# Optimization experiments

Measured on AMD Instinct MI355X. Metric: run time of the kernel, lower is better.

Reference implementation:

```python
import jax, jax.numpy as jnp
import numpy as np
import math

B, S, F, D = 8, 2048, 1024, 1024
NEG = -1e9


def setup_inputs() -> dict:
    key = jax.random.key(0)
    ks = jax.random.split(key, 5)
    x = jax.random.normal(ks[0], (B, S, F), dtype=jnp.float32)
    r_mat = jax.random.normal(ks[1], (B, S, S), dtype=jnp.float32)
    # shared causal attention mask [S, S] (1 = keep, 0 = masked)
    attn_mask = jnp.tril(jnp.ones((S, S), dtype=jnp.float32))
    # per-batch padding mask [B, 1, S]: last 128 tokens of half the batch padded
    pad = jnp.ones((B, 1, S), dtype=jnp.float32)
    pad = pad.at[B // 2:, :, S - 128:].set(0.0)
    Wq = jax.random.normal(ks[2], (F, D), dtype=jnp.float32) / math.sqrt(F)
    Wk = jax.random.normal(ks[3], (F, D), dtype=jnp.float32) / math.sqrt(F)
    Wv = jax.random.normal(ks[4], (F, D), dtype=jnp.float32) / math.sqrt(F)
    return {"x": x, "r_mat": r_mat, "attn_mask": attn_mask, "pad_mask": pad,
            "Wq": Wq, "Wk": Wk, "Wv": Wv}


def reference(x, r_mat, attn_mask, pad_mask, Wq, Wk, Wv):
    scale = math.sqrt(x.shape[-1])  # original scales by sqrt(features)
    q = jnp.einsum('bsf,fd->bsd', x, Wq)
    k = jnp.einsum('bsf,fd->bsd', x, Wk)
    v = jnp.einsum('bsf,fd->bsd', x, Wv)
    scores = jnp.einsum('bsd,btd->bst', q, k) / scale  # [B, S, S]
    keep = (pad_mask != 0.0) & (attn_mask[None] != 0.0)  # [B, S, S] broadcast
    r = jnp.where(keep, r_mat, NEG)
    r = jax.nn.softmax(r, axis=-1)
    scores = jnp.where(keep, scores + r, NEG)
    prob = jax.nn.softmax(scores, axis=-1)
    return jnp.einsum('bst,btd->bsd', prob, v)
```

## Files before the change

kernel.cpp:

```cpp
#include <hip/hip_runtime.h>
#include <hip/hip_bf16.h>

#define B_ 8
#define S_ 2048
#define F_ 1024
#define D_ 1024
#define TRI_ 136
#define TELEM_ 16384

typedef unsigned short u16;
typedef float f32x4 __attribute__((ext_vector_type(4)));
typedef __bf16 bf16x8 __attribute__((ext_vector_type(8)));
typedef unsigned short u16x8 __attribute__((ext_vector_type(8)));

__device__ __forceinline__ u16 f2bf(float f) {
  union { float f; unsigned u; } v; v.f = f;
  unsigned r = v.u + 0x7fff + ((v.u >> 16) & 1);
  return (u16)(r >> 16);
}
__device__ __forceinline__ float bf2f(u16 b) {
  union { unsigned u; float f; } v; v.u = ((unsigned)b) << 16;
  return v.f;
}

__device__ __forceinline__ void stage16(const u16* g, u16* l) {
  __builtin_amdgcn_global_load_lds(
      (const __attribute__((address_space(1))) void*)g,
      (__attribute__((address_space(3))) void*)l, 16, 0, 0);
}

__device__ __forceinline__ int xcd_swz(int f, int n) {
  int per = n >> 3;
  return (f & 7) * per + (f >> 3);
}


__global__ __launch_bounds__(256) void prep(const float* __restrict__ x,
                                            const float* __restrict__ Wq,
                                            const float* __restrict__ Wk,
                                            const float* __restrict__ Wv,
                                            u16* __restrict__ xb,
                                            u16* __restrict__ Wt) {
  __shared__ float tile[32][33];
  if (blockIdx.x < 2048) {
    int n4 = (B_ * S_ * F_) / 4;
    for (int i = blockIdx.x * 256 + threadIdx.x; i < n4; i += 2048 * 256) {
      float4 v = ((const float4*)x)[i];
      ushort4 o;
      o.x = f2bf(v.x); o.y = f2bf(v.y); o.z = f2bf(v.z); o.w = f2bf(v.w);
      ((ushort4*)xb)[i] = o;
    }
  } else {
    int f = blockIdx.x - 2048;
    int z = f >> 10;
    int f2 = f & 1023;
    int f0 = (f2 >> 5) * 32, d0 = (f2 & 31) * 32;
    const float* W = (z == 0) ? Wq : ((z == 1) ? Wk : Wv);
    int tx = threadIdx.x & 31, ty = threadIdx.x >> 5;
    for (int i = 0; i < 4; i++)
      tile[ty + i * 8][tx] = W[(size_t)(f0 + ty + i * 8) * D_ + d0 + tx];
    __syncthreads();
    u16* o = Wt + (size_t)z * D_ * F_;
    for (int i = 0; i < 4; i++)
      o[(size_t)(d0 + ty + i * 8) * F_ + f0 + tx] = f2bf(tile[tx][ty + i * 8]);
  }
}

__global__ __launch_bounds__(256) void er_pass(const float* __restrict__ r,
                                               const float* __restrict__ pm,
                                               u16* __restrict__ er,
                                               float* __restrict__ rowsum) {
  int row = blockIdx.x;
  int b = row >> 11, s = row & 2047;
  if (threadIdx.x == 0) rowsum[row] = 0.f;
  const float4* rp = (const float4*)(r + (size_t)row * S_);
  const float4* pp = (const float4*)(pm + (size_t)b * S_);
  int nk = (s >> 2) + 1;
  int nw = ((s >> 7) + 1) << 5;
  float4 ev[8];
  float acc = 0.f;
  #pragma unroll
  for (int it = 0; it < 8; it++) {
    int i = threadIdx.x + it * 256;
    if (i < nk) {
      float4 rv = rp[i], pv = pp[i];
      int t0 = i << 2;
      float4 e;
      #pragma unroll
      for (int j = 0; j < 4; j++) {
        bool keep = (t0 + j <= s) && ((&pv.x)[j] != 0.f);
        (&e.x)[j] = keep ? __expf((&rv.x)[j] - 16.f) : 0.f;
        acc += (&e.x)[j];
      }
      ev[it] = e;
    }
  }
  for (int off = 1; off < 64; off <<= 1) acc += __shfl_xor(acc, off);
  __shared__ float wsum[4];
  int lane = threadIdx.x & 63, w = threadIdx.x >> 6;
  if (lane == 0) wsum[w] = acc;
  __syncthreads();
  float invr = 1.f / (wsum[0] + wsum[1] + wsum[2] + wsum[3]);
  int c = s >> 7, rin = s & 127;
  u16* tb = er + (size_t)(b * TRI_ + c * (c + 1) / 2) * TELEM_ + rin * 128;
  #pragma unroll
  for (int it = 0; it < 8; it++) {
    int i = threadIdx.x + it * 256;
    if (i < nw) {
      int t0 = i << 2;
      float4 pv = pp[i];
      ushort4 o;
      #pragma unroll
      for (int j = 0; j < 4; j++) {
        bool keep = (t0 + j <= s) && ((&pv.x)[j] != 0.f);
        float val = keep ? (&ev[it].x)[j] * invr : -1e9f;
        (&o.x)[j] = f2bf(val);
      }
      *(ushort4*)(tb + (size_t)(t0 >> 7) * TELEM_ + (t0 & 127)) = o;
    }
  }
}

__global__ __launch_bounds__(256) void r_rowsum(const float* __restrict__ r,
                                                const float* __restrict__ pm,
                                                float* __restrict__ rs) {
  int row = blockIdx.x;
  int b = row >> 11, s = row & 2047;
  const float4* rp = (const float4*)(r + (size_t)row * S_);
  const float4* pp = (const float4*)(pm + (size_t)b * S_);
  int nv = (s >> 2) + 1;
  float acc = 0.f;
  for (int i = threadIdx.x; i < nv; i += 256) {
    float4 rv = rp[i];
    float4 pv = pp[i];
    int t0 = i << 2;
    #pragma unroll
    for (int j = 0; j < 4; j++) {
      int t = t0 + j;
      if (t <= s && (&pv.x)[j] != 0.f) acc += __expf((&rv.x)[j] - 16.f);
    }
  }
  for (int off = 1; off < 64; off <<= 1) acc += __shfl_xor(acc, off);
  __shared__ float wsum[4];
  int lane = threadIdx.x & 63, w = threadIdx.x >> 6;
  if (lane == 0) wsum[w] = acc;
  __syncthreads();
  if (threadIdx.x == 0) rs[row] = wsum[0] + wsum[1] + wsum[2] + wsum[3];
}


__device__ __forceinline__ bf16x8 readfrag(const u16* lds, int row, int ks, int hi) {
  int c = ((ks << 6) + (hi << 4)) ^ ((row & 7) << 4);
  return *(const bf16x8*)((const char*)lds + row * 128 + c);
}

#define SYNC_POINT()                                                             \
  __builtin_amdgcn_sched_barrier(0);                                             \
  __builtin_amdgcn_s_barrier();                                                  \
  __builtin_amdgcn_sched_barrier(0);


__device__ __forceinline__ void stageA(const u16* __restrict__ src, int ld, int h,
                                       u16* ldsA, int w, int l) {
  int base = ((w >> 2) * 128) + h * 64 + ((w & 3) * 16);
  int r = l >> 3, ch = (l & 7) ^ (l >> 3);
  #pragma unroll
  for (int i = 0; i < 2; i++) {
    int row = base + i * 8;
    stage16(src + (size_t)(row + r) * ld + ch * 8, ldsA + row * 64);
  }
}
__device__ __forceinline__ void stageB(const u16* __restrict__ src, int ld, int h,
                                       u16* ldsB, int w, int l) {
  int base = h * 128 + w * 16;
  int r = l >> 3, ch = (l & 7) ^ (l >> 3);
  #pragma unroll
  for (int i = 0; i < 2; i++) {
    int row = base + i * 8;
    stage16(src + (size_t)(row + r) * ld + ch * 8, ldsB + row * 64);
  }
}

#define MFMAQ(AF, KB, MB)                                                        \
  __builtin_amdgcn_s_setprio(1);                                                 \
  _Pragma("unroll")                                                              \
  for (int m = 0; m < 4; m++)                                                    \
    _Pragma("unroll")                                                            \
    for (int n = 0; n < 4; n++)                                                  \
      acc[(MB) + m][n] = __builtin_amdgcn_mfma_f32_16x16x32_bf16(                \
          AF[m], bfr[(KB) + n], acc[(MB) + m][n], 0, 0, 0);                      \
  __builtin_amdgcn_s_setprio(0);

__device__ __forceinline__ void gemm256(const u16* __restrict__ A, int lda,
                                        const u16* __restrict__ B, int ldb,
                                        int nT, u16* lds, f32x4 acc[8][4]) {
  const int t = threadIdx.x, w = t >> 6, l = t & 63;
  const int wr = w >> 2, wc = w & 3;
  u16* A0 = lds;           u16* B0 = lds + 16384;
  u16* A1 = lds + 32768;   u16* B1 = lds + 49152;

  #pragma unroll
  for (int m = 0; m < 8; m++)
    #pragma unroll
    for (int n = 0; n < 4; n++)
      #pragma unroll
      for (int j = 0; j < 4; j++) acc[m][n][j] = 0.f;

  stageB(B, ldb, 0, B0, w, l);
  stageB(B, ldb, 1, B0, w, l);
  stageA(A, lda, 0, A0, w, l);
  stageA(A, lda, 1, A0, w, l);
  if (nT > 1) stageA(A + 64, lda, 0, A1, w, l);
  asm volatile("s_waitcnt vmcnt(4)" ::: "memory");
  SYNC_POINT()

  const int arow = wr * 128 + (l & 15), hi = l >> 4;
  const int brow = wc * 64 + (l & 15);

  for (int kt = 0; kt < nT; kt++) {
    u16* cA = (kt & 1) ? A1 : A0;
    u16* cB = (kt & 1) ? B1 : B0;
    u16* nA = (kt & 1) ? A0 : A1;
    u16* nB = (kt & 1) ? B0 : B1;
    const u16* An1 = A + (size_t)(kt + 1) * 64;
    const u16* Bn1 = B + (size_t)(kt + 1) * 64;
    const u16* An2 = A + (size_t)(kt + 2) * 64;
    const bool has1 = (kt + 1 < nT), has2 = (kt + 2 < nT);
    bf16x8 af0[4], af1[4], bfr[8];

    #pragma unroll
    for (int m = 0; m < 4; m++) af0[m] = readfrag(cA, arow + m * 16, 0, hi);
    #pragma unroll
    for (int n = 0; n < 4; n++) bfr[n] = readfrag(cB, brow + n * 16, 0, hi);
    #pragma unroll
    for (int m = 0; m < 4; m++) af1[m] = readfrag(cA, arow + m * 16, 1, hi);
    #pragma unroll
    for (int n = 0; n < 4; n++) bfr[4 + n] = readfrag(cB, brow + n * 16, 1, hi);
    if (has1) stageB(Bn1, ldb, 0, nB, w, l);
    MFMAQ(af0, 0, 0)

    if (has1) {
      stageB(Bn1, ldb, 1, nB, w, l);
      asm volatile("s_waitcnt vmcnt(4)" ::: "memory");
    } else {
      asm volatile("s_waitcnt vmcnt(0)" ::: "memory");
    }
    SYNC_POINT()
    MFMAQ(af1, 4, 0)

    #pragma unroll
    for (int m = 0; m < 4; m++) af0[m] = readfrag(cA, arow + 64 + m * 16, 0, hi);
    #pragma unroll
    for (int m = 0; m < 4; m++) af1[m] = readfrag(cA, arow + 64 + m * 16, 1, hi);
    if (has2) stageA(An2, lda, 0, cA, w, l);
    MFMAQ(af0, 0, 4)

    if (has1) stageA(An1, lda, 1, nA, w, l);
    if (has1 && has2)  { asm volatile("s_waitcnt vmcnt(4)" ::: "memory"); }
    else if (has1)     { asm volatile("s_waitcnt vmcnt(2)" ::: "memory"); }
    else               { asm volatile("s_waitcnt vmcnt(0)" ::: "memory"); }
    SYNC_POINT()
    MFMAQ(af1, 4, 4)
  }
}

__device__ __forceinline__ void store256_bf16(f32x4 acc[8][4], u16* smem,
                                              u16* dst, int ld) {
  int t = threadIdx.x, w = t >> 6, l = t & 63;
  int wr = w >> 2, wc = w & 3;
  #pragma unroll
  for (int q = 0; q < 4; q++) {
    __syncthreads();
    if (wr == (q >> 1)) {
      int mb = (q & 1) * 4;
      #pragma unroll
      for (int mm = 0; mm < 4; mm++)
        #pragma unroll
        for (int j = 0; j < 4; j++) {
          int row = mm * 16 + (l >> 4) * 4 + j;
          #pragma unroll
          for (int n = 0; n < 4; n++)
            smem[row * 264 + wc * 64 + n * 16 + (l & 15)] = f2bf(acc[mb + mm][n][j]);
        }
    }
    __syncthreads();
    #pragma unroll
    for (int i = 0; i < 4; i++) {
      int idx = i * 512 + t;
      int row = idx >> 5, ch = idx & 31;
      *(u16x8*)(dst + (size_t)(q * 64 + row) * ld + ch * 8) =
          *(const u16x8*)(smem + row * 264 + ch * 8);
    }
  }
}

__global__ __launch_bounds__(512, 2) void gemm_qkv(
    const u16* __restrict__ xb, const u16* __restrict__ Wt,
    u16* __restrict__ qb, u16* __restrict__ kb, u16* __restrict__ vT) {
  __shared__ __align__(16) u16 lds[65536];
  int z = blockIdx.z;
  f32x4 acc[8][4];
  if (z < 2) {
    int m0 = blockIdx.x * 256, n0 = blockIdx.y * 256;
    gemm256(xb + (size_t)m0 * F_, F_,
            Wt + (size_t)z * D_ * F_ + (size_t)n0 * F_, F_, F_ / 64, lds, acc);
    store256_bf16(acc, lds, ((z == 0) ? qb : kb) + (size_t)m0 * D_ + n0, D_);
  } else {
    int d0 = blockIdx.y * 256, s0g = blockIdx.x * 256;
    gemm256(Wt + 2ULL * D_ * F_ + (size_t)d0 * F_, F_,
            xb + (size_t)s0g * F_, F_, F_ / 64, lds, acc);
    int b = s0g >> 11, s0 = s0g & 2047;
    store256_bf16(acc, lds, vT + (size_t)b * D_ * S_ + (size_t)d0 * S_ + s0, S_);
  }
}


template <int PACKA>
__device__ __forceinline__ void gemm128(const u16* __restrict__ A, int lda,
                                        const u16* __restrict__ B, int ldb,
                                        int nT, u16* lds, f32x4 acc[4][4]) {
  const int t = threadIdx.x, w = t >> 6, l = t & 63;
  const int wr = w >> 1, wc = w & 1;
  u16* A0 = lds;          u16* B0 = lds + 8192;
  u16* A1 = lds + 16384;  u16* B1 = lds + 24576;

  auto asrc = [&](int kt) -> const u16* {
    return PACKA ? A + (size_t)(kt >> 1) * TELEM_ + (kt & 1) * 64
                 : A + (size_t)kt * 64;
  };

  #pragma unroll
  for (int m = 0; m < 4; m++)
    #pragma unroll
    for (int n = 0; n < 4; n++)
      #pragma unroll
      for (int j = 0; j < 4; j++) acc[m][n][j] = 0.f;

  auto stg = [&](const u16* src, int ld, int h, u16* dst) {
    int base = h * 64 + w * 16;
    int r = l >> 3, ch = (l & 7) ^ (l >> 3);
    #pragma unroll
    for (int i = 0; i < 2; i++) {
      int row = base + i * 8;
      stage16(src + (size_t)(row + r) * ld + ch * 8, dst + row * 64);
    }
  };

  stg(asrc(0), PACKA ? 128 : lda, 0, A0);
  stg(asrc(0), PACKA ? 128 : lda, 1, A0);
  stg(B, ldb, 0, B0);
  stg(B, ldb, 1, B0);
  if (nT > 1) {
    stg(asrc(1), PACKA ? 128 : lda, 0, A1);
    stg(asrc(1), PACKA ? 128 : lda, 1, A1);
    asm volatile("s_waitcnt vmcnt(4)" ::: "memory");
  } else {
    asm volatile("s_waitcnt vmcnt(0)" ::: "memory");
  }
  SYNC_POINT()

  const int arow = wr * 64 + (l & 15), brow = wc * 64 + (l & 15), hi = l >> 4;

  for (int kt = 0; kt < nT; kt++) {
    u16* cA = (kt & 1) ? A1 : A0;
    u16* cB = (kt & 1) ? B1 : B0;
    u16* nB = (kt & 1) ? B0 : B1;
    const bool has1 = (kt + 1 < nT), has2 = (kt + 2 < nT);
    bf16x8 a0f[4], b0f[4], a1f[4], b1f[4];

    #pragma unroll
    for (int m = 0; m < 4; m++) a0f[m] = readfrag(cA, arow + m * 16, 0, hi);
    #pragma unroll
    for (int n = 0; n < 4; n++) b0f[n] = readfrag(cB, brow + n * 16, 0, hi);
    #pragma unroll
    for (int m = 0; m < 4; m++) a1f[m] = readfrag(cA, arow + m * 16, 1, hi);
    #pragma unroll
    for (int n = 0; n < 4; n++) b1f[n] = readfrag(cB, brow + n * 16, 1, hi);
    if (has1) {
      stg(B + (size_t)(kt + 1) * 64, ldb, 0, nB);
      stg(B + (size_t)(kt + 1) * 64, ldb, 1, nB);
    }
    __builtin_amdgcn_s_setprio(1);
    #pragma unroll
    for (int m = 0; m < 4; m++)
      #pragma unroll
      for (int n = 0; n < 4; n++)
        acc[m][n] = __builtin_amdgcn_mfma_f32_16x16x32_bf16(a0f[m], b0f[n], acc[m][n], 0, 0, 0);
    __builtin_amdgcn_s_setprio(0);
    asm volatile("s_waitcnt lgkmcnt(0)" ::: "memory");
    SYNC_POINT()

    if (has2) {
      stg(asrc(kt + 2), PACKA ? 128 : lda, 0, cA);
      stg(asrc(kt + 2), PACKA ? 128 : lda, 1, cA);
    }
    __builtin_amdgcn_s_setprio(1);
    #pragma unroll
    for (int m = 0; m < 4; m++)
      #pragma unroll
      for (int n = 0; n < 4; n++)
        acc[m][n] = __builtin_amdgcn_mfma_f32_16x16x32_bf16(a1f[m], b1f[n], acc[m][n], 0, 0, 0);
    __builtin_amdgcn_s_setprio(0);
    if (has2)      { asm volatile("s_waitcnt vmcnt(4)" ::: "memory"); }
    else if (has1) { asm volatile("s_waitcnt vmcnt(0)" ::: "memory"); }
    SYNC_POINT()
  }
}

__device__ __forceinline__ void tri_decode(int x, int& mt, int& nt) {
  mt = (int)((sqrtf(8.f * x + 1.f) - 1.f) * 0.5f);
  while ((mt + 1) * (mt + 2) / 2 <= x) mt++;
  while (mt * (mt + 1) / 2 > x) mt--;
  nt = x - mt * (mt + 1) / 2;
}

__global__ __launch_bounds__(256, 2) void attn_scores_er(
    const u16* __restrict__ qb, const u16* __restrict__ kb,
    const u16* __restrict__ er, u16* __restrict__ P,
    float* __restrict__ rowsum) {
  __shared__ __align__(16) u16 lds[32768];
  int f = xcd_swz(blockIdx.x + 136 * blockIdx.y, 1088);
  int x = f % 136, b = f / 136;
  int mt, nt; tri_decode(x, mt, nt);
  int m0 = mt * 128, n0 = nt * 128;
  f32x4 acc[4][4];
  gemm128<0>(qb + ((size_t)b * S_ + m0) * D_, D_,
             kb + ((size_t)b * S_ + n0) * D_, D_, D_ / 64, lds, acc);
  int t = threadIdx.x, w = t >> 6, l = t & 63;
  int wr = w >> 1, wc = w & 1;
  float* fs = (float*)lds;
  size_t tbase = (size_t)(b * TRI_ + mt * (mt + 1) / 2 + nt) * TELEM_;
  #pragma unroll
  for (int h = 0; h < 2; h++) {
    __syncthreads();
    if (wr == h) {
      #pragma unroll
      for (int m = 0; m < 4; m++)
        #pragma unroll
        for (int j = 0; j < 4; j++) {
          int row = m * 16 + (l >> 4) * 4 + j;
          #pragma unroll
          for (int n = 0; n < 4; n++)
            fs[row * 132 + wc * 64 + n * 16 + (l & 15)] = acc[m][n][j];
        }
    }
    __syncthreads();
    int row = t >> 2, cg = t & 3;
    int rin = h * 64 + row;
    const u16* et = er + tbase + (size_t)rin * 128 + cg * 32;
    u16* pt = P + tbase + (size_t)rin * 128 + cg * 32;
    const float* fsc = fs + row * 132 + cg * 32;
    float rsum = 0.f;
    #pragma unroll
    for (int cc = 0; cc < 4; cc++) {
      int ch = (cg + cc) & 3;
      f32x4 q0 = *(const f32x4*)(fsc + ch * 8);
      f32x4 q1 = *(const f32x4*)(fsc + ch * 8 + 4);
      u16x8 e8 = *(const u16x8*)(et + ch * 8);
      u16x8 o;
      #pragma unroll
      for (int k = 0; k < 8; k++) {
        float qk = (k < 4) ? q0[k] : q1[k - 4];
        float e = __expf(fmaf(qk, 0.03125f, bf2f(e8[k]) - 16.f));
        u16 pb = f2bf(e); o[k] = pb; rsum += bf2f(pb);
      }
      *(u16x8*)(pt + ch * 8) = o;
    }
    rsum += __shfl_xor(rsum, 1);
    rsum += __shfl_xor(rsum, 2);
    if ((t & 3) == 0) atomicAdd(&rowsum[b * S_ + m0 + rin], rsum);
  }
}

__global__ __launch_bounds__(256, 2) void attn_scores_rm(
    const u16* __restrict__ qb, const u16* __restrict__ kb,
    const float* __restrict__ r_mat, const float* __restrict__ pm,
    const float* __restrict__ rs_r, u16* __restrict__ P,
    float* __restrict__ rowsum) {
  __shared__ __align__(16) u16 lds[32768];
  int f = xcd_swz(blockIdx.x + 136 * blockIdx.y, 1088);
  int x = f % 136, b = f / 136;
  int mt, nt; tri_decode(x, mt, nt);
  int m0 = mt * 128, n0 = nt * 128;
  f32x4 acc[4][4];
  gemm128<0>(qb + ((size_t)b * S_ + m0) * D_, D_,
             kb + ((size_t)b * S_ + n0) * D_, D_, D_ / 64, lds, acc);
  int t = threadIdx.x, w = t >> 6, l = t & 63;
  int wr = w >> 1, wc = w & 1;
  float* fs = (float*)lds;
  const float* rb = r_mat + (size_t)b * S_ * S_;
  const float* pmp = pm + (size_t)b * S_ + n0;
  size_t tbase = (size_t)(b * TRI_ + mt * (mt + 1) / 2 + nt) * TELEM_;
  #pragma unroll
  for (int h = 0; h < 2; h++) {
    __syncthreads();
    if (wr == h) {
      #pragma unroll
      for (int m = 0; m < 4; m++)
        #pragma unroll
        for (int j = 0; j < 4; j++) {
          int row = m * 16 + (l >> 4) * 4 + j;
          #pragma unroll
          for (int n = 0; n < 4; n++)
            fs[row * 132 + wc * 64 + n * 16 + (l & 15)] = acc[m][n][j];
        }
    }
    __syncthreads();
    int row = t >> 2, cg = t & 3;
    int srow = m0 + h * 64 + row;
    float invr = 1.f / rs_r[b * S_ + srow];
    const float* rrow = rb + (size_t)srow * S_ + n0 + cg * 32;
    u16* pt = P + tbase + (size_t)(h * 64 + row) * 128 + cg * 32;
    const float* fsc = fs + row * 132 + cg * 32;
    float rsum = 0.f;
    #pragma unroll
    for (int cc = 0; cc < 4; cc++) {
      int ch = (cg + cc) & 3;
      f32x4 q0 = *(const f32x4*)(fsc + ch * 8);
      f32x4 q1 = *(const f32x4*)(fsc + ch * 8 + 4);
      f32x4 r0 = *(const f32x4*)(rrow + ch * 8);
      f32x4 r1 = *(const f32x4*)(rrow + ch * 8 + 4);
      f32x4 p0 = *(const f32x4*)(pmp + cg * 32 + ch * 8);
      f32x4 p1 = *(const f32x4*)(pmp + cg * 32 + ch * 8 + 4);
      u16x8 o;
      #pragma unroll
      for (int k = 0; k < 8; k++) {
        int tc = n0 + cg * 32 + ch * 8 + k;
        float rv = (k < 4) ? r0[k] : r1[k - 4];
        float pmv = (k < 4) ? p0[k] : p1[k - 4];
        float qk = (k < 4) ? q0[k] : q1[k - 4];
        bool keep = (tc <= srow) && (pmv != 0.f);
        float rsm = __expf(rv - 16.f) * invr;
        float e = keep ? __expf(fmaf(qk, 0.03125f, rsm - 16.f)) : 0.f;
        u16 pb = f2bf(e); o[k] = pb; rsum += bf2f(pb);
      }
      *(u16x8*)(pt + ch * 8) = o;
    }
    rsum += __shfl_xor(rsum, 1);
    rsum += __shfl_xor(rsum, 2);
    if ((t & 3) == 0) atomicAdd(&rowsum[b * S_ + srow], rsum);
  }
}

__global__ __launch_bounds__(256, 2) void attn_pv(
    const u16* __restrict__ P, const u16* __restrict__ vT,
    const float* __restrict__ rowsum, float* __restrict__ out) {
  __shared__ __align__(16) u16 lds[32768];
  int f = xcd_swz(blockIdx.x + 16 * blockIdx.y + 128 * blockIdx.z, 1024);
  int mt = 15 - (f & 15), dt = (f >> 4) & 7, b = f >> 7;
  int m0 = mt * 128, n0 = dt * 128;
  int nT = 2 * (mt + 1);
  f32x4 acc[4][4];
  gemm128<1>(P + (size_t)(b * TRI_ + mt * (mt + 1) / 2) * TELEM_, 128,
             vT + ((size_t)b * D_ + n0) * S_, S_, nT, lds, acc);
  int t = threadIdx.x, w = t >> 6, l = t & 63;
  int wr = w >> 1, wc = w & 1;
  float* fs = (float*)lds;
  #pragma unroll
  for (int h = 0; h < 2; h++) {
    __syncthreads();
    if (wr == h) {
      #pragma unroll
      for (int m = 0; m < 4; m++)
        #pragma unroll
        for (int j = 0; j < 4; j++) {
          int row = m * 16 + (l >> 4) * 4 + j;
          float inv = 1.f / rowsum[b * S_ + m0 + h * 64 + row];
          #pragma unroll
          for (int n = 0; n < 4; n++)
            fs[row * 132 + wc * 64 + n * 16 + (l & 15)] = acc[m][n][j] * inv;
        }
    }
    __syncthreads();
    #pragma unroll
    for (int i = 0; i < 8; i++) {
      int idx = i * 256 + t;
      int row = idx >> 5, c4 = (idx & 31) << 2;
      *(float4*)(out + ((size_t)b * S_ + m0 + h * 64 + row) * D_ + n0 + c4) =
          *(const float4*)(fs + row * 132 + c4);
    }
  }
}

extern "C" void kernel_launch(void* const* d_in, const int* in_sizes, int n_in,
                              void* d_out, int out_size, void* d_ws, size_t ws_size,
                              hipStream_t stream) {
  const float* x     = (const float*)d_in[0];
  const float* r_mat = (const float*)d_in[1];
  const float* pm    = (const float*)d_in[3];
  const float* Wq    = (const float*)d_in[4];
  const float* Wk    = (const float*)d_in[5];
  const float* Wv    = (const float*)d_in[6];
  float* out = (float*)d_out;
  char* ws = (char*)d_ws;

  const size_t PK = (size_t)B_ * TRI_ * TELEM_ * 2;
  u16*   qb     = (u16*)(ws + 0);
  u16*   kb     = (u16*)(ws + 33554432ULL);
  u16*   vT     = (u16*)(ws + 67108864ULL);
  float* rowsum = (float*)(ws + 100663296ULL);
  float* rs_r   = (float*)(ws + 100728832ULL);
  u16*   xb     = (u16*)(ws + 100794368ULL);
  u16*   Wt     = (u16*)(ws + 134348800ULL);
  u16*   er     = (u16*)(ws + 100794368ULL);
  bool use_er   = ws_size >= 100794368ULL + 2 * PK;
  u16*   P      = use_er ? (u16*)(ws + 100794368ULL + PK)
                         : (u16*)(ws + 100794368ULL);

  prep<<<dim3(5120), dim3(256), 0, stream>>>(x, Wq, Wk, Wv, xb, Wt);
  if (!use_er)
    r_rowsum<<<dim3(B_ * S_), dim3(256), 0, stream>>>(r_mat, pm, rs_r);
  gemm_qkv<<<dim3(64, 4, 3), dim3(512), 0, stream>>>(xb, Wt, qb, kb, vT);
  if (use_er) {
    er_pass<<<dim3(B_ * S_), dim3(256), 0, stream>>>(r_mat, pm, er, rowsum);
    attn_scores_er<<<dim3(136, 8), dim3(256), 0, stream>>>(qb, kb, er, P, rowsum);
  } else {
    hipMemsetAsync(rowsum, 0, B_ * S_ * sizeof(float), stream);
    attn_scores_rm<<<dim3(136, 8), dim3(256), 0, stream>>>(qb, kb, r_mat, pm, rs_r, P, rowsum);
  }
  attn_pv<<<dim3(16, 8, 8), dim3(256), 0, stream>>>(P, vT, rowsum, out);
}
```

Baseline: 273.2 us.

## Use 256x256 tiles for causal scores and pair PV row tiles per block

The QK^T scores kernel now uses 512-thread blocks that compute 256x256 tiles with a gemm256 routine over 36 triangular super-tiles per batch. It then scatters the valid 128x128 subtiles into the packed triangular P layout. This raises operand reuse and cuts the number of blocks, at the cost of computing the above-diagonal 128x128 subtile in each diagonal super-tile. The PV kernel now assigns each block a long and a short causal row tile (mt and 15-mt) so work per block is balanced, and it launches half as many blocks.

```diff
diff --git a/kernel.cpp b/kernel.cpp
--- a/kernel.cpp
+++ b/kernel.cpp
@@ -414,61 +414,71 @@
   nt = x - mt * (mt + 1) / 2;
 }
 
-__global__ __launch_bounds__(256, 2) void attn_scores_er(
+__global__ __launch_bounds__(512, 2) void attn_scores_er(
     const u16* __restrict__ qb, const u16* __restrict__ kb,
     const u16* __restrict__ er, u16* __restrict__ P,
     float* __restrict__ rowsum) {
-  __shared__ __align__(16) u16 lds[32768];
-  int f = xcd_swz(blockIdx.x + 136 * blockIdx.y, 1088);
-  int x = f % 136, b = f / 136;
-  int mt, nt; tri_decode(x, mt, nt);
-  int m0 = mt * 128, n0 = nt * 128;
-  f32x4 acc[4][4];
-  gemm128<0>(qb + ((size_t)b * S_ + m0) * D_, D_,
-             kb + ((size_t)b * S_ + n0) * D_, D_, D_ / 64, lds, acc);
+  __shared__ __align__(16) u16 lds[65536];
+  int f = xcd_swz(blockIdx.x + 36 * blockIdx.y, 288);
+  int x = f % 36, b = f / 36;
+  int MT, NT; tri_decode(x, MT, NT);
+  int m0 = MT * 256, n0 = NT * 256;
+  f32x4 acc[8][4];
+  gemm256(qb + ((size_t)b * S_ + m0) * D_, D_,
+          kb + ((size_t)b * S_ + n0) * D_, D_, D_ / 64, lds, acc);
   int t = threadIdx.x, w = t >> 6, l = t & 63;
-  int wr = w >> 1, wc = w & 1;
+  int wr = w >> 2, wc = w & 3;
   float* fs = (float*)lds;
-  size_t tbase = (size_t)(b * TRI_ + mt * (mt + 1) / 2 + nt) * TELEM_;
-  #pragma unroll
-  for (int h = 0; h < 2; h++) {
-    __syncthreads();
-    if (wr == h) {
-      #pragma unroll
-      for (int m = 0; m < 4; m++)
+  const u16* erb = er + (size_t)b * TRI_ * TELEM_;
+  u16* Pb = P + (size_t)b * TRI_ * TELEM_;
+  #pragma unroll
+  for (int q = 0; q < 4; q++) {
+    __syncthreads();
+    if (wr == (q >> 1)) {
+      int mb = (q & 1) * 4;
+      #pragma unroll
+      for (int mm = 0; mm < 4; mm++)
         #pragma unroll
         for (int j = 0; j < 4; j++) {
-          int row = m * 16 + (l >> 4) * 4 + j;
+          int row = mm * 16 + (l >> 4) * 4 + j;
           #pragma unroll
           for (int n = 0; n < 4; n++)
-            fs[row * 132 + wc * 64 + n * 16 + (l & 15)] = acc[m][n][j];
+            fs[row * 260 + wc * 64 + n * 16 + (l & 15)] = acc[mb + mm][n][j];
         }
     }
     __syncthreads();
-    int row = t >> 2, cg = t & 3;
-    int rin = h * 64 + row;
-    const u16* et = er + tbase + (size_t)rin * 128 + cg * 32;
-    u16* pt = P + tbase + (size_t)rin * 128 + cg * 32;
-    const float* fsc = fs + row * 132 + cg * 32;
+    int row = t >> 3, cg = t & 7;
+    int rin256 = q * 64 + row;
+    int mt128 = 2 * MT + (rin256 >> 7), rin128 = rin256 & 127;
+    int nt128 = 2 * NT + (cg >> 2);
+    bool valid = (nt128 <= mt128);
     float rsum = 0.f;
-    #pragma unroll
-    for (int cc = 0; cc < 4; cc++) {
-      int ch = (cg + cc) & 3;
-      f32x4 q0 = *(const f32x4*)(fsc + ch * 8);
-      f32x4 q1 = *(const f32x4*)(fsc + ch * 8 + 4);
-      u16x8 e8 = *(const u16x8*)(et + ch * 8);
-      u16x8 o;
-      #pragma unroll
-      for (int k = 0; k < 8; k++) {
-        float qk = (k < 4) ? q0[k] : q1[k - 4];
-        float e = __expf(fmaf(qk, 0.03125f, bf2f(e8[k]) - 16.f));
-        u16 pb = f2bf(e); o[k] = pb; rsum += bf2f(pb);
+    if (valid) {
+      size_t sb = (size_t)(mt128 * (mt128 + 1) / 2 + nt128) * TELEM_
+                  + (size_t)rin128 * 128 + (cg & 3) * 32;
+      const u16* et = erb + sb;
+      u16* pt = Pb + sb;
+      const float* fsc = fs + row * 260 + cg * 32;
+      #pragma unroll
+      for (int cc = 0; cc < 4; cc++) {
+        int ch = (cg + cc) & 3;
+        f32x4 q0 = *(const f32x4*)(fsc + ch * 8);
+        f32x4 q1 = *(const f32x4*)(fsc + ch * 8 + 4);
+        u16x8 e8 = *(const u16x8*)(et + ch * 8);
+        u16x8 o;
+        #pragma unroll
+        for (int k = 0; k < 8; k++) {
+          float qk = (k < 4) ? q0[k] : q1[k - 4];
+          float e = __expf(fmaf(qk, 0.03125f, bf2f(e8[k]) - 16.f));
+          u16 pb = f2bf(e); o[k] = pb; rsum += bf2f(pb);
+        }
+        *(u16x8*)(pt + ch * 8) = o;
       }
-      *(u16x8*)(pt + ch * 8) = o;
     }
     rsum += __shfl_xor(rsum, 1);
     rsum += __shfl_xor(rsum, 2);
-    if ((t & 3) == 0) atomicAdd(&rowsum[b * S_ + m0 + rin], rsum);
+    rsum += __shfl_xor(rsum, 4);
+    if ((t & 7) == 0) atomicAdd(&rowsum[b * S_ + m0 + rin256], rsum);
   }
 }
 
@@ -546,39 +556,43 @@
     const u16* __restrict__ P, const u16* __restrict__ vT,
     const float* __restrict__ rowsum, float* __restrict__ out) {
   __shared__ __align__(16) u16 lds[32768];
-  int f = xcd_swz(blockIdx.x + 16 * blockIdx.y + 128 * blockIdx.z, 1024);
-  int mt = 15 - (f & 15), dt = (f >> 4) & 7, b = f >> 7;
-  int m0 = mt * 128, n0 = dt * 128;
-  int nT = 2 * (mt + 1);
-  f32x4 acc[4][4];
-  gemm128<1>(P + (size_t)(b * TRI_ + mt * (mt + 1) / 2) * TELEM_, 128,
-             vT + ((size_t)b * D_ + n0) * S_, S_, nT, lds, acc);
-  int t = threadIdx.x, w = t >> 6, l = t & 63;
-  int wr = w >> 1, wc = w & 1;
-  float* fs = (float*)lds;
-  #pragma unroll
-  for (int h = 0; h < 2; h++) {
-    __syncthreads();
-    if (wr == h) {
-      #pragma unroll
-      for (int m = 0; m < 4; m++)
+  int f = xcd_swz(blockIdx.x + 8 * blockIdx.y + 64 * blockIdx.z, 512);
+  int mtp = f & 7, dt = (f >> 3) & 7, b = f >> 6;
+  for (int hf = 0; hf < 2; hf++) {
+    int mt = hf ? mtp : (15 - mtp);
+    int m0 = mt * 128, n0 = dt * 128;
+    int nT = 2 * (mt + 1);
+    f32x4 acc[4][4];
+    gemm128<1>(P + (size_t)(b * TRI_ + mt * (mt + 1) / 2) * TELEM_, 128,
+               vT + ((size_t)b * D_ + n0) * S_, S_, nT, lds, acc);
+    int t = threadIdx.x, w = t >> 6, l = t & 63;
+    int wr = w >> 1, wc = w & 1;
+    float* fs = (float*)lds;
+    #pragma unroll
+    for (int h = 0; h < 2; h++) {
+      __syncthreads();
+      if (wr == h) {
         #pragma unroll
-        for (int j = 0; j < 4; j++) {
-          int row = m * 16 + (l >> 4) * 4 + j;
-          float inv = 1.f / rowsum[b * S_ + m0 + h * 64 + row];
+        for (int m = 0; m < 4; m++)
           #pragma unroll
-          for (int n = 0; n < 4; n++)
-            fs[row * 132 + wc * 64 + n * 16 + (l & 15)] = acc[m][n][j] * inv;
-        }
-    }
-    __syncthreads();
-    #pragma unroll
-    for (int i = 0; i < 8; i++) {
-      int idx = i * 256 + t;
-      int row = idx >> 5, c4 = (idx & 31) << 2;
-      *(float4*)(out + ((size_t)b * S_ + m0 + h * 64 + row) * D_ + n0 + c4) =
-          *(const float4*)(fs + row * 132 + c4);
-    }
+          for (int j = 0; j < 4; j++) {
+            int row = m * 16 + (l >> 4) * 4 + j;
+            float inv = 1.f / rowsum[b * S_ + m0 + h * 64 + row];
+            #pragma unroll
+            for (int n = 0; n < 4; n++)
+              fs[row * 132 + wc * 64 + n * 16 + (l & 15)] = acc[m][n][j] * inv;
+          }
+      }
+      __syncthreads();
+      #pragma unroll
+      for (int i = 0; i < 8; i++) {
+        int idx = i * 256 + t;
+        int row = idx >> 5, c4 = (idx & 31) << 2;
+        *(float4*)(out + ((size_t)b * S_ + m0 + h * 64 + row) * D_ + n0 + c4) =
+            *(const float4*)(fs + row * 132 + c4);
+      }
+    }
+    __syncthreads();
   }
 }
 
@@ -613,10 +627,10 @@
   gemm_qkv<<<dim3(64, 4, 3), dim3(512), 0, stream>>>(xb, Wt, qb, kb, vT);
   if (use_er) {
     er_pass<<<dim3(B_ * S_), dim3(256), 0, stream>>>(r_mat, pm, er, rowsum);
-    attn_scores_er<<<dim3(136, 8), dim3(256), 0, stream>>>(qb, kb, er, P, rowsum);
+    attn_scores_er<<<dim3(36, 8), dim3(512), 0, stream>>>(qb, kb, er, P, rowsum);
   } else {
     hipMemsetAsync(rowsum, 0, B_ * S_ * sizeof(float), stream);
     attn_scores_rm<<<dim3(136, 8), dim3(256), 0, stream>>>(qb, kb, r_mat, pm, rs_r, P, rowsum);
   }
-  attn_pv<<<dim3(16, 8, 8), dim3(256), 0, stream>>>(P, vT, rowsum, out);
-}
+  attn_pv<<<dim3(8, 8, 8), dim3(256), 0, stream>>>(P, vT, rowsum, out);
+}
```

Result: no change. 268.0 us (median of 3 runs) (-1.9%).
